# Performance work log

Measured on AMD Instinct MI355X. Metric: run time of the kernel, lower is better.

The kernel has to match this reference:

```python
import jax, jax.numpy as jnp
import numpy as np

N5, N4, N3, K = 10242, 2562, 642, 7  # icosphere node counts (levels 5,4,3), spatial kernel size
M = 32  # mchannel
EPS = 1e-8


def _sconv(x, neigh, W, b, relu=True):
    # x: [B,T,N,Cin]; neigh: [N,K] 1-ring indices; W: [K,Cin,Cout]
    xn = x[:, :, neigh, :]                        # [B,T,N,K,Cin] irregular gather
    y = jnp.einsum('btnkc,kcd->btnd', xn, W) + b  # per-node kernel contraction
    return jax.nn.relu(y) if relu else y


def _spool(x, pidx):
    # max-pool fine->coarse mesh: pidx [Ncoarse,Kp] indexes fine nodes
    return jnp.max(x[:, :, pidx, :], axis=3)


def _unpool(x, uidx):
    # coarse->fine copy: uidx [Nfine] indexes coarse nodes
    return x[:, :, uidx, :]


def _cos(f, a):
    # torch.nn.CosineSimilarity(dim=-1): dot / max(|f|*|a|, eps)
    dot = jnp.sum(f * a, axis=-1)
    nf = jnp.linalg.norm(f, axis=-1)
    na = jnp.linalg.norm(a, axis=-1)
    return dot / jnp.maximum(nf * na, EPS)


def setup_inputs() -> dict:
    key = jax.random.key(0)
    ks = jax.random.split(key, 32)
    w = lambda i, shape: jax.random.normal(ks[i], shape, jnp.float32) * 0.05
    inp = {
        'frame': jax.random.normal(ks[0], (1, 16, N5, 3), jnp.float32),
        'aem': jax.random.normal(ks[1], (1, 16, N5), jnp.float32),
        'W0f': w(2, (K, 3, M)),        'b0f': w(3, (M,)),
        'W0a': w(4, (K, 1, M)),        'b0a': w(5, (M,)),
        'W1f': w(6, (K, M, 2 * M)),    'b1f': w(7, (2 * M,)),
        'W1a': w(8, (K, M, 2 * M)),    'b1a': w(9, (2 * M,)),
        'W2f': w(10, (K, 2 * M, 4 * M)), 'b2f': w(11, (4 * M,)),
        'W2a': w(12, (K, 2 * M, 4 * M)), 'b2a': w(13, (4 * M,)),
        'W7': w(14, (K, 12 * M, 2 * M)), 'b7': w(15, (2 * M,)),
        'W8': w(16, (K, 4 * M, M)),    'b8': w(17, (M,)),
        'W9': w(18, (K, M, 1)),        'b9': w(19, (1,)),
        'neigh5': jax.random.randint(ks[20], (N5, K), 0, N5),
        'neigh4': jax.random.randint(ks[21], (N4, K), 0, N4),
        'neigh3': jax.random.randint(ks[22], (N3, K), 0, N3),
        'pool5': jax.random.randint(ks[23], (N4, K), 0, N5),
        'pool4': jax.random.randint(ks[24], (N3, K), 0, N4),
        'up4': jax.random.randint(ks[25], (N4,), 0, N3),
        'up5': jax.random.randint(ks[26], (N5,), 0, N4),
        'Tlocation': jax.random.randint(ks[27], (1, 16), 0, 16),
    }
    return inp


def reference(frame, aem, W0f, b0f, W0a, b0a, W1f, b1f, W1a, b1a, W2f, b2f,
              W2a, b2a, W7, b7, W8, b8, W9, b9,
              neigh5, neigh4, neigh3, pool5, pool4, up4, up5, Tlocation):
    a = aem[..., None]                                    # [B,T,N5,1]
    # encoder level 0 (N5)
    c0f = _sconv(frame, neigh5, W0f, b0f)
    c0a = _sconv(a, neigh5, W0a, b0a)
    p0f = _spool(c0f, pool5)
    p0a = _spool(c0a, pool5)
    m0 = _cos(c0f, c0a)[..., None]                        # [B,T,N5,1]
    c0f_att, c0a_att = c0f * m0, c0a * m0
    # encoder level 1 (N4)
    c1f = _sconv(p0f, neigh4, W1f, b1f)
    c1a = _sconv(p0a, neigh4, W1a, b1a)
    p1f = _spool(c1f, pool4)
    p1a = _spool(c1a, pool4)
    m1 = _cos(c1f, c1a)[..., None]
    c1f_att, c1a_att = c1f * m1, c1a * m1
    # bottleneck (N3)
    c2f = _sconv(p1f, neigh3, W2f, b2f)
    c2a = _sconv(p1a, neigh3, W2a, b2a)
    m2 = _cos(c2f, c2a)[..., None]
    conv2 = jnp.concatenate((c2f * m2, c2a * m2), axis=-1)  # [B,T,N3,8M]
    # decoder
    cat7 = jnp.concatenate((_unpool(conv2, up4), c1f_att, c1a_att), axis=-1)  # [B,T,N4,12M]
    conv7 = _sconv(cat7, neigh4, W7, b7)
    cat8 = jnp.concatenate((_unpool(conv7, up5), c0f_att, c0a_att), axis=-1)  # [B,T,N5,4M]
    conv8 = _sconv(cat8, neigh5, W8, b8)
    conv9 = _sconv(conv8, neigh5, W9, b9, relu=False)[..., 0]  # [B,T,N5]
    return jax.nn.softmax(conv9, axis=-1)
```

## Files before the change

kernel.cpp:

```cpp
#include <hip/hip_runtime.h>
#include <cfloat>
#include <cstdint>


constexpr int T  = 16;
constexpr int n5 = 10242, n4 = 2562, n3 = 642;
constexpr int K  = 7;

using bf16x8 = __attribute__((ext_vector_type(8))) short;
using f32x4  = __attribute__((ext_vector_type(4))) float;

static __device__ __forceinline__ float bf2f(unsigned short u) {
    return __uint_as_float((unsigned)u << 16);
}
static __device__ __forceinline__ unsigned short f2bf(float x) {
    unsigned u = __float_as_uint(x);
    u += 0x7FFF + ((u >> 16) & 1);
    return (unsigned short)(u >> 16);
}

__global__ __launch_bounds__(256) void conv0_kernel(
    const float* __restrict__ frame, const float* __restrict__ aem,
    const float* __restrict__ W0f, const float* __restrict__ b0f,
    const float* __restrict__ W0a, const float* __restrict__ b0a,
    const int* __restrict__ neigh5,
    unsigned short* __restrict__ c0f, unsigned short* __restrict__ c0a,
    unsigned short* __restrict__ att0)
{
    const int g = threadIdx.x >> 5;
    const int d = threadIdx.x & 31;
    const int per_t = (n5 + 7) / 8;
    const int t = blockIdx.x / per_t;
    const int n = (blockIdx.x % per_t) * 8 + g;
    if (n >= n5) return;

    float accf = b0f[d];
    float acca = b0a[d];
    const int* nb = neigh5 + n * K;
    #pragma unroll
    for (int k = 0; k < K; ++k) {
        const int j = nb[k];
        const float* fr = frame + ((size_t)t * n5 + j) * 3;
        const float av = aem[(size_t)t * n5 + j];
        accf = fmaf(fr[0], W0f[(k * 3 + 0) * 32 + d], accf);
        accf = fmaf(fr[1], W0f[(k * 3 + 1) * 32 + d], accf);
        accf = fmaf(fr[2], W0f[(k * 3 + 2) * 32 + d], accf);
        acca = fmaf(av, W0a[k * 32 + d], acca);
    }
    accf = fmaxf(accf, 0.f);
    acca = fmaxf(acca, 0.f);

    float dot = accf * acca, ff = accf * accf, aa = acca * acca;
    #pragma unroll
    for (int m = 1; m < 32; m <<= 1) {
        dot += __shfl_xor(dot, m, 32);
        ff  += __shfl_xor(ff,  m, 32);
        aa  += __shfl_xor(aa,  m, 32);
    }
    const float mm = dot / fmaxf(sqrtf(ff) * sqrtf(aa), 1e-8f);
    const size_t base = ((size_t)t * n5 + n) * 32;
    c0f[base + d] = f2bf(accf);
    c0a[base + d] = f2bf(acca);
    const size_t abase = ((size_t)t * n5 + n) * 64;
    att0[abase + d]      = f2bf(accf * mm);
    att0[abase + 32 + d] = f2bf(acca * mm);
}

template<int C>
__global__ __launch_bounds__(256) void pool_kernel(
    const unsigned short* __restrict__ in, const int* __restrict__ pidx,
    int Nin, int Nout, unsigned short* __restrict__ out)
{
    constexpr int C8 = C / 8;
    const int idx = blockIdx.x * 256 + threadIdx.x;
    if (idx >= T * Nout * C8) return;
    const int c8 = idx % C8;
    const int n  = (idx / C8) % Nout;
    const int t  = idx / (C8 * Nout);
    const int* pp = pidx + n * K;
    float m[8];
    #pragma unroll
    for (int j = 0; j < 8; ++j) m[j] = -FLT_MAX;
    #pragma unroll
    for (int k = 0; k < K; ++k) {
        const uint4 v = reinterpret_cast<const uint4*>(in)[((size_t)t * Nin + pp[k]) * C8 + c8];
        const unsigned short* s = reinterpret_cast<const unsigned short*>(&v);
        #pragma unroll
        for (int j = 0; j < 8; ++j) m[j] = fmaxf(m[j], bf2f(s[j]));
    }
    unsigned short o[8];
    #pragma unroll
    for (int j = 0; j < 8; ++j) o[j] = f2bf(m[j]);
    reinterpret_cast<uint4*>(out)[((size_t)t * Nout + n) * C8 + c8] =
        *reinterpret_cast<const uint4*>(o);
}

template<int C, int NN>
__global__ __launch_bounds__(256) void cosatt_kernel(
    const unsigned short* __restrict__ f, const unsigned short* __restrict__ a,
    unsigned short* __restrict__ att)
{
    constexpr int CPL = C / 64;
    const int w = threadIdx.x >> 6, lane = threadIdx.x & 63;
    const int idx = blockIdx.x * 4 + w;
    if (idx >= T * NN) return;
    const unsigned short* fr = f + (size_t)idx * C;
    const unsigned short* ar = a + (size_t)idx * C;
    float xs[CPL], ys[CPL];
    float dot = 0.f, ff = 0.f, aa = 0.f;
    #pragma unroll
    for (int i = 0; i < CPL; ++i) {
        const float x = bf2f(fr[lane + i * 64]);
        const float y = bf2f(ar[lane + i * 64]);
        xs[i] = x; ys[i] = y;
        dot = fmaf(x, y, dot);
        ff  = fmaf(x, x, ff);
        aa  = fmaf(y, y, aa);
    }
    #pragma unroll
    for (int msk = 1; msk < 64; msk <<= 1) {
        dot += __shfl_xor(dot, msk);
        ff  += __shfl_xor(ff,  msk);
        aa  += __shfl_xor(aa,  msk);
    }
    const float m = dot / fmaxf(sqrtf(ff) * sqrtf(aa), 1e-8f);
    unsigned short* orow = att + (size_t)idx * 2 * C;
    #pragma unroll
    for (int i = 0; i < CPL; ++i) {
        orow[lane + i * 64]     = f2bf(xs[i] * m);
        orow[C + lane + i * 64] = f2bf(ys[i] * m);
    }
}

struct PlainB16 {
    const uint4* x; int N; int C8;
    struct Ref { int o; };
    __device__ __forceinline__ Ref prep(int t, int node) const {
        return { (int)(((size_t)t * N + node) * C8) };
    }
    __device__ __forceinline__ uint4 chunk(const Ref& r, int c8) const {
        return x[r.o + c8];
    }
};

struct Cat7B16 {
    const uint4* att2; const uint4* att1; const int* up4;
    __device__ __forceinline__ uint4 row8(int t, int node, int c8) const {
        if (c8 < 32)
            return att2[((size_t)t * n3 + up4[node]) * 32 + c8];
        return att1[((size_t)t * n4 + node) * 16 + (c8 - 32)];
    }
};

struct Cat8B16 {
    const uint4* cv7; const uint4* att0; const int* up5;
    __device__ __forceinline__ uint4 row8(int t, int node, int c8) const {
        if (c8 < 8)
            return cv7[((size_t)t * n4 + up5[node]) * 8 + c8];
        return att0[((size_t)t * n5 + node) * 8 + (c8 - 8)];
    }
};

__global__ __launch_bounds__(256) void wprep_all_kernel(
    const float* __restrict__ W1f, const float* __restrict__ W1a,
    const float* __restrict__ W2f, const float* __restrict__ W2a,
    const float* __restrict__ W7,  const float* __restrict__ W8,
    unsigned short* __restrict__ Wt1f, unsigned short* __restrict__ Wt1a,
    unsigned short* __restrict__ Wt2f, unsigned short* __restrict__ Wt2a,
    unsigned short* __restrict__ Wt7,  unsigned short* __restrict__ Wt8)
{
    int idx = blockIdx.x * 256 + threadIdx.x;
    const float* W; unsigned short* Wt; int KCv, CO;
    if (idx < 14336)       { W = W1f; Wt = Wt1f; KCv = 224;  CO = 64;  }
    else if (idx < 28672)  { idx -= 14336;  W = W1a; Wt = Wt1a; KCv = 224;  CO = 64;  }
    else if (idx < 86016)  { idx -= 28672;  W = W2f; Wt = Wt2f; KCv = 448;  CO = 128; }
    else if (idx < 143360) { idx -= 86016;  W = W2a; Wt = Wt2a; KCv = 448;  CO = 128; }
    else if (idx < 315392) { idx -= 143360; W = W7;  Wt = Wt7;  KCv = 2688; CO = 64;  }
    else                   { idx -= 315392; W = W8;  Wt = Wt8;  KCv = 896;  CO = 32;  }
    const int d = idx / KCv, kc = idx - d * KCv;
    Wt[idx] = f2bf(W[(size_t)kc * CO + d]);
}

template<int CIN, int COUT, int BM, class Loader>
__global__ __launch_bounds__(256) void gemm_zp_kernel(
    Loader ldr, int N, int Mt,
    const unsigned short* __restrict__ Wt,
    unsigned short* __restrict__ Z)
{
    constexpr int KC    = K * CIN;
    constexpr int BK    = 64;
    constexpr int KSTEPS = CIN / BK;
    constexpr int U4R   = BK / 8;
    constexpr int WGR_N = COUT / 32;
    constexpr int WGR_M = 4 / WGR_N;
    constexpr int VPTA  = BM * U4R / 256;
    constexpr int VPTW  = COUT * U4R / 256;
    static_assert(BM == WGR_M * 32 && CIN % BK == 0 && VPTW >= 1 && BM * COUT <= BM * BK);

    __shared__ __align__(16) unsigned short As[BM * BK];
    __shared__ __align__(16) unsigned short Ws[COUT * BK];

    const int xcd = blockIdx.x & 7;
    int rest = blockIdx.x >> 3;
    const int half = Mt * K;
    const int hi = (rest >= half) ? 1 : 0;
    const int t  = 2 * xcd + hi;
    const int j  = rest - hi * half;
    const int tile_m = j / K;
    const int kk_    = j % K;

    const int tid = threadIdx.x, lane = tid & 63, wave = tid >> 6;
    const int wr = wave / WGR_N, wc = wave % WGR_N;
    const int l15 = lane & 15, lhi = lane >> 4;
    const int m0 = tile_m * BM;

    f32x4 acc[2][2] = {};

    for (int ks = 0; ks < KSTEPS; ++ks) {
        uint4 av[VPTA];
        #pragma unroll
        for (int v = 0; v < VPTA; ++v) {
            const int g = tid + v * 256, row = g / U4R, c8 = g % U4R;
            av[v] = ldr.row8(t, min(m0 + row, N - 1), ks * U4R + c8);
        }
        uint4 wv[VPTW];
        #pragma unroll
        for (int v = 0; v < VPTW; ++v) {
            const int g = tid + v * 256, d = g / U4R, c8 = g % U4R;
            wv[v] = *reinterpret_cast<const uint4*>(
                Wt + (size_t)d * KC + kk_ * CIN + ks * BK + c8 * 8);
        }

        __syncthreads();
        #pragma unroll
        for (int v = 0; v < VPTA; ++v) {
            const int g = tid + v * 256, row = g / U4R, c8 = g % U4R;
            *reinterpret_cast<uint4*>(&As[(row * BK + c8 * 8) ^ ((row & 7) << 3)]) = av[v];
        }
        #pragma unroll
        for (int v = 0; v < VPTW; ++v) {
            const int g = tid + v * 256, d = g / U4R, c8 = g % U4R;
            *reinterpret_cast<uint4*>(&Ws[(d * BK + c8 * 8) ^ ((d & 7) << 3)]) = wv[v];
        }
        __syncthreads();

        #pragma unroll
        for (int kk2 = 0; kk2 < 2; ++kk2) {
            const int kb = kk2 * 32 + lhi * 8;
            bf16x8 a[2], b[2];
            #pragma unroll
            for (int m = 0; m < 2; ++m) {
                const int row = wr * 32 + m * 16 + l15;
                a[m] = *reinterpret_cast<const bf16x8*>(&As[(row * BK + kb) ^ ((row & 7) << 3)]);
            }
            #pragma unroll
            for (int n = 0; n < 2; ++n) {
                const int col = wc * 32 + n * 16 + l15;
                b[n] = *reinterpret_cast<const bf16x8*>(&Ws[(col * BK + kb) ^ ((col & 7) << 3)]);
            }
            #pragma unroll
            for (int m = 0; m < 2; ++m)
                #pragma unroll
                for (int n = 0; n < 2; ++n)
                    acc[m][n] = __builtin_amdgcn_mfma_f32_16x16x32_bf16(a[m], b[n], acc[m][n], 0, 0, 0);
        }
    }

    __syncthreads();
    unsigned short* Cs = As;
    #pragma unroll
    for (int n = 0; n < 2; ++n) {
        const int col = wc * 32 + n * 16 + l15;
        #pragma unroll
        for (int m = 0; m < 2; ++m)
            #pragma unroll
            for (int i = 0; i < 4; ++i)
                Cs[(wr * 32 + m * 16 + lhi * 4 + i) * COUT + col] = f2bf(acc[m][n][i]);
    }
    __syncthreads();
    constexpr int RPT = COUT / 8;
    constexpr int CV  = BM * COUT / 8 / 256;
    #pragma unroll
    for (int v = 0; v < CV; ++v) {
        const int g = tid + v * 256, row = g / RPT, c8 = g % RPT;
        const int grow = m0 + row;
        if (grow < N)
            *reinterpret_cast<uint4*>(
                &Z[(((size_t)kk_ * T + t) * N + grow) * COUT + c8 * 8]) =
                *reinterpret_cast<const uint4*>(&Cs[row * COUT + c8 * 8]);
    }
}

template<int COUT>
__global__ __launch_bounds__(256) void epi_p_kernel(
    const unsigned short* __restrict__ Z, const int* __restrict__ neigh,
    int N, int Bt, const float* __restrict__ bias, unsigned short* __restrict__ out)
{
    constexpr int C8 = COUT / 8;
    const int xcd = blockIdx.x & 7;
    int idx = blockIdx.x >> 3;
    const int hi = (idx >= Bt) ? 1 : 0;
    const int t  = 2 * xcd + hi;
    const int e  = (idx - hi * Bt) * 256 + threadIdx.x;
    if (e >= N * C8) return;
    const int c8 = e % C8;
    const int n  = e / C8;
    const int* nb = neigh + n * K;

    float s[8];
    #pragma unroll
    for (int j = 0; j < 8; ++j) s[j] = bias[c8 * 8 + j];
    #pragma unroll
    for (int k = 0; k < K; ++k) {
        const uint4 v = *reinterpret_cast<const uint4*>(
            &Z[(((size_t)k * T + t) * N + nb[k]) * COUT + c8 * 8]);
        const unsigned short* p = reinterpret_cast<const unsigned short*>(&v);
        #pragma unroll
        for (int j = 0; j < 8; ++j) s[j] += bf2f(p[j]);
    }
    unsigned short o[8];
    #pragma unroll
    for (int j = 0; j < 8; ++j) o[j] = f2bf(fmaxf(s[j], 0.f));
    *reinterpret_cast<uint4*>(&out[((size_t)t * N + n) * COUT + c8 * 8]) =
        *reinterpret_cast<const uint4*>(o);
}

template<int CIN, int COUT, class Loader>
__device__ __forceinline__ void sconv_tile(
    const Loader& ldr, const int* __restrict__ neigh, int N, int t,
    int tile_m, int tile_n,
    const unsigned short* __restrict__ Wt, const float* __restrict__ bias,
    unsigned short* __restrict__ out)
{
    constexpr int KC     = K * CIN;
    constexpr int CHUNKS = CIN / 32;
    constexpr int STEPS  = K * CHUNKS;
    constexpr int D      = STEPS < 3 ? STEPS : 3;

    const int lane = threadIdx.x & 63;
    const int l15 = lane & 15, lhi = lane >> 4;

    const int r0 = tile_m * 32 + l15;
    const int row0 = min(r0, N - 1), row1 = min(r0 + 16, N - 1);

    typename Loader::Ref ref0[K], ref1[K];
    #pragma unroll
    for (int k = 0; k < K; ++k) {
        ref0[k] = ldr.prep(t, neigh[row0 * K + k]);
        ref1[k] = ldr.prep(t, neigh[row1 * K + k]);
    }

    const int col0 = tile_n * 32 + l15;
    const unsigned short* w0p = Wt + (size_t)col0 * KC + lhi * 8;
    const unsigned short* w1p = w0p + (size_t)16 * KC;

    uint4 qa0[D], qa1[D], qb0[D], qb1[D];

    auto issue = [&](int s, int slot) {
        const int k = s / CHUNKS, c = s - k * CHUNKS;
        const int c8 = c * 4 + lhi;
        qa0[slot] = ldr.chunk(ref0[k], c8);
        qa1[slot] = ldr.chunk(ref1[k], c8);
        qb0[slot] = *reinterpret_cast<const uint4*>(w0p + k * CIN + c * 32);
        qb1[slot] = *reinterpret_cast<const uint4*>(w1p + k * CIN + c * 32);
    };

    f32x4 acc[2][2] = {};

    #pragma unroll
    for (int s = 0; s < D; ++s) issue(s, s);
    __builtin_amdgcn_sched_barrier(0);

    #pragma unroll
    for (int s = 0; s < STEPS; ++s) {
        const int slot = s % D;
        const bf16x8 a0 = __builtin_bit_cast(bf16x8, qa0[slot]);
        const bf16x8 a1 = __builtin_bit_cast(bf16x8, qa1[slot]);
        const bf16x8 b0 = __builtin_bit_cast(bf16x8, qb0[slot]);
        const bf16x8 b1 = __builtin_bit_cast(bf16x8, qb1[slot]);
        acc[0][0] = __builtin_amdgcn_mfma_f32_16x16x32_bf16(a0, b0, acc[0][0], 0, 0, 0);
        acc[0][1] = __builtin_amdgcn_mfma_f32_16x16x32_bf16(a0, b1, acc[0][1], 0, 0, 0);
        acc[1][0] = __builtin_amdgcn_mfma_f32_16x16x32_bf16(a1, b0, acc[1][0], 0, 0, 0);
        acc[1][1] = __builtin_amdgcn_mfma_f32_16x16x32_bf16(a1, b1, acc[1][1], 0, 0, 0);
        if (s + D < STEPS) issue(s + D, slot);
        __builtin_amdgcn_sched_barrier(0);
    }

    #pragma unroll
    for (int n = 0; n < 2; ++n) {
        const int gcol = tile_n * 32 + n * 16 + l15;
        const float bv = bias[gcol];
        #pragma unroll
        for (int m = 0; m < 2; ++m) {
            #pragma unroll
            for (int i = 0; i < 4; ++i) {
                const int grow = tile_m * 32 + m * 16 + lhi * 4 + i;
                if (grow < N)
                    out[((size_t)t * N + grow) * COUT + gcol] =
                        f2bf(fmaxf(acc[m][n][i] + bv, 0.f));
            }
        }
    }
}

template<int CIN, int COUT, class Loader>
__global__ __launch_bounds__(64, 2) void sconv_rd2_kernel(
    Loader lf, Loader la, const int* __restrict__ neigh, int N, int U,
    const unsigned short* __restrict__ Wtf, const unsigned short* __restrict__ Wta,
    const float* __restrict__ bf_, const float* __restrict__ ba_,
    unsigned short* __restrict__ of_, unsigned short* __restrict__ oa_)
{
    constexpr int TN = COUT / 32;
    const int xcd = blockIdx.x & 7;
    int idx = blockIdx.x >> 3;
    const int sel = idx & 1; idx >>= 1;
    const int hi = (idx >= U) ? 1 : 0;
    const int t  = 2 * xcd + hi;
    const int w  = idx - hi * U;
    const Loader L = sel ? la : lf;
    const unsigned short* Wt = sel ? Wta : Wtf;
    const float* bias = sel ? ba_ : bf_;
    unsigned short* out = sel ? oa_ : of_;
    sconv_tile<CIN, COUT, Loader>(L, neigh, N, t, w / TN, w % TN, Wt, bias, out);
}

__global__ __launch_bounds__(256) void conv9_kernel(
    const unsigned short* __restrict__ cv8, const int* __restrict__ neigh5,
    const float* __restrict__ W9, const float* __restrict__ b9,
    float* __restrict__ logits)
{
    const int idx = blockIdx.x * 256 + threadIdx.x;
    if (idx >= T * n5) return;
    const int n = idx % n5;
    const int t = idx / n5;
    float acc = b9[0];
    const int* nb = neigh5 + n * K;
    #pragma unroll
    for (int k = 0; k < K; ++k) {
        const uint4* row = reinterpret_cast<const uint4*>(cv8 + ((size_t)t * n5 + nb[k]) * 32);
        const float* wk = W9 + k * 32;
        #pragma unroll
        for (int c4 = 0; c4 < 4; ++c4) {
            const uint4 v = row[c4];
            const unsigned short* s = reinterpret_cast<const unsigned short*>(&v);
            #pragma unroll
            for (int jj = 0; jj < 8; ++jj)
                acc = fmaf(bf2f(s[jj]), wk[c4 * 8 + jj], acc);
        }
    }
    logits[idx] = acc;
}

__global__ __launch_bounds__(1024) void softmax_kernel(
    const float* __restrict__ logits, float* __restrict__ out)
{
    const int t = blockIdx.x, tid = threadIdx.x;
    const float* x = logits + (size_t)t * n5;
    float* y = out + (size_t)t * n5;
    __shared__ float redmax[16], redsum[16];

    float mx = -FLT_MAX;
    for (int i = tid; i < n5; i += 1024) mx = fmaxf(mx, x[i]);
    #pragma unroll
    for (int m = 1; m < 64; m <<= 1) mx = fmaxf(mx, __shfl_xor(mx, m));
    if ((tid & 63) == 0) redmax[tid >> 6] = mx;
    __syncthreads();
    mx = redmax[0];
    #pragma unroll
    for (int i = 1; i < 16; ++i) mx = fmaxf(mx, redmax[i]);

    float s = 0.f;
    for (int i = tid; i < n5; i += 1024) s += expf(x[i] - mx);
    #pragma unroll
    for (int m = 1; m < 64; m <<= 1) s += __shfl_xor(s, m);
    if ((tid & 63) == 0) redsum[tid >> 6] = s;
    __syncthreads();
    s = 0.f;
    #pragma unroll
    for (int i = 0; i < 16; ++i) s += redsum[i];

    for (int i = tid; i < n5; i += 1024) y[i] = expf(x[i] - mx) / s;
}

extern "C" void kernel_launch(void* const* d_in, const int* in_sizes, int n_in,
                              void* d_out, int out_size, void* d_ws, size_t ws_size,
                              hipStream_t stream)
{
    const float* frame = (const float*)d_in[0];
    const float* aem   = (const float*)d_in[1];
    const float* W0f = (const float*)d_in[2];
    const float* b0f = (const float*)d_in[3];
    const float* W0a = (const float*)d_in[4];
    const float* b0a = (const float*)d_in[5];
    const float* W1f = (const float*)d_in[6];
    const float* b1f = (const float*)d_in[7];
    const float* W1a = (const float*)d_in[8];
    const float* b1a = (const float*)d_in[9];
    const float* W2f = (const float*)d_in[10];
    const float* b2f = (const float*)d_in[11];
    const float* W2a = (const float*)d_in[12];
    const float* b2a = (const float*)d_in[13];
    const float* W7  = (const float*)d_in[14];
    const float* b7  = (const float*)d_in[15];
    const float* W8  = (const float*)d_in[16];
    const float* b8  = (const float*)d_in[17];
    const float* W9  = (const float*)d_in[18];
    const float* b9  = (const float*)d_in[19];
    const int* neigh5 = (const int*)d_in[20];
    const int* neigh4 = (const int*)d_in[21];
    const int* neigh3 = (const int*)d_in[22];
    const int* pool5  = (const int*)d_in[23];
    const int* pool4  = (const int*)d_in[24];
    const int* up4    = (const int*)d_in[25];
    const int* up5    = (const int*)d_in[26];

    unsigned short* wsu = (unsigned short*)d_ws;
    size_t off = 0;
    auto ua = [&](size_t n) {
        unsigned short* p = wsu + off; off += (n + 63) & ~(size_t)63; return p;
    };
    unsigned short* c0f  = ua((size_t)T * n5 * 32);
    unsigned short* c0a  = ua((size_t)T * n5 * 32);
    unsigned short* att0 = ua((size_t)T * n5 * 64);
    unsigned short* p0f  = ua((size_t)T * n4 * 32);
    unsigned short* p0a  = ua((size_t)T * n4 * 32);
    unsigned short* c1f  = ua((size_t)T * n4 * 64);
    unsigned short* c1a  = ua((size_t)T * n4 * 64);
    unsigned short* att1 = ua((size_t)T * n4 * 128);
    unsigned short* p1f  = ua((size_t)T * n3 * 64);
    unsigned short* p1a  = ua((size_t)T * n3 * 64);
    unsigned short* c2f  = ua((size_t)T * n3 * 128);
    unsigned short* c2a  = ua((size_t)T * n3 * 128);
    unsigned short* att2 = ua((size_t)T * n3 * 256);
    unsigned short* cv7  = ua((size_t)T * n4 * 64);
    unsigned short* cv8  = ua((size_t)T * n5 * 32);
    unsigned short* Wt1f = ua((size_t)64 * 224);
    unsigned short* Wt1a = ua((size_t)64 * 224);
    unsigned short* Wt2f = ua((size_t)128 * 448);
    unsigned short* Wt2a = ua((size_t)128 * 448);
    unsigned short* Wt7  = ua((size_t)64 * 2688);
    unsigned short* Wt8  = ua((size_t)32 * 896);
    unsigned short* Zbuf = ua((size_t)K * T * n5 * 32);
    float* lgt = (float*)(wsu + ((off + 1) & ~(size_t)1));

    wprep_all_kernel<<<1344, 256, 0, stream>>>(
        W1f, W1a, W2f, W2a, W7, W8, Wt1f, Wt1a, Wt2f, Wt2a, Wt7, Wt8);

    conv0_kernel<<<T * ((n5 + 7) / 8), 256, 0, stream>>>(
        frame, aem, W0f, b0f, W0a, b0a, neigh5, c0f, c0a, att0);

    {
        const int thr = T * n4 * (32 / 8);
        pool_kernel<32><<<(thr + 255) / 256, 256, 0, stream>>>(c0f, pool5, n5, n4, p0f);
        pool_kernel<32><<<(thr + 255) / 256, 256, 0, stream>>>(c0a, pool5, n5, n4, p0a);
    }

    {
        constexpr int U = 81 * 2;
        sconv_rd2_kernel<32, 64><<<8 * 4 * U, 64, 0, stream>>>(
            PlainB16{(const uint4*)p0f, n4, 4}, PlainB16{(const uint4*)p0a, n4, 4},
            neigh4, n4, U, Wt1f, Wt1a, b1f, b1a, c1f, c1a);
    }
    cosatt_kernel<64, n4><<<(T * n4 + 3) / 4, 256, 0, stream>>>(c1f, c1a, att1);

    {
        const int thr = T * n3 * (64 / 8);
        pool_kernel<64><<<(thr + 255) / 256, 256, 0, stream>>>(c1f, pool4, n4, n3, p1f);
        pool_kernel<64><<<(thr + 255) / 256, 256, 0, stream>>>(c1a, pool4, n4, n3, p1a);
    }

    {
        constexpr int U = 21 * 4;
        sconv_rd2_kernel<64, 128><<<8 * 4 * U, 64, 0, stream>>>(
            PlainB16{(const uint4*)p1f, n3, 8}, PlainB16{(const uint4*)p1a, n3, 8},
            neigh3, n3, U, Wt2f, Wt2a, b2f, b2a, c2f, c2a);
    }
    cosatt_kernel<128, n3><<<(T * n3 + 3) / 4, 256, 0, stream>>>(c2f, c2a, att2);

    {
        constexpr int Mt = (n4 + 63) / 64;
        gemm_zp_kernel<384, 64, 64><<<16 * Mt * K, 256, 0, stream>>>(
            Cat7B16{(const uint4*)att2, (const uint4*)att1, up4}, n4, Mt, Wt7, Zbuf);
        constexpr int Bt = (n4 * 8 + 255) / 256;
        epi_p_kernel<64><<<8 * 2 * Bt, 256, 0, stream>>>(
            Zbuf, neigh4, n4, Bt, b7, cv7);
    }

    {
        constexpr int Mt = (n5 + 127) / 128;
        gemm_zp_kernel<128, 32, 128><<<16 * Mt * K, 256, 0, stream>>>(
            Cat8B16{(const uint4*)cv7, (const uint4*)att0, up5}, n5, Mt, Wt8, Zbuf);
        constexpr int Bt = (n5 * 4 + 255) / 256;
        epi_p_kernel<32><<<8 * 2 * Bt, 256, 0, stream>>>(
            Zbuf, neigh5, n5, Bt, b8, cv8);
    }

    conv9_kernel<<<(T * n5 + 255) / 256, 256, 0, stream>>>(cv8, neigh5, W9, b9, lgt);

    softmax_kernel<<<T, 1024, 0, stream>>>(lgt, (float*)d_out);
}
```

Measured before the change: 265.4 us.

## Stage activation tile once in LDS and loop over all kernel taps per block

The gather-then-GEMM kernels for conv7 and conv8 now load the whole activation tile (all Cin) into shared memory once per block and loop over the seven kernel taps inside the block. Previously each tap was a separate block that reloaded the same activation rows. Weights are now read straight from global memory into registers instead of being staged through LDS. This cuts redundant gather traffic and the grid size by a factor of K, at the cost of more LDS per block (lower occupancy for CIN=384), fewer blocks, and uncoalesced, uncached-in-LDS weight loads.

```diff
diff --git a/kernel.cpp b/kernel.cpp
--- a/kernel.cpp
+++ b/kernel.cpp
@@ -145,19 +145,25 @@
 
 struct Cat7B16 {
     const uint4* att2; const uint4* att1; const int* up4;
-    __device__ __forceinline__ uint4 row8(int t, int node, int c8) const {
-        if (c8 < 32)
-            return att2[((size_t)t * n3 + up4[node]) * 32 + c8];
-        return att1[((size_t)t * n4 + node) * 16 + (c8 - 32)];
+    struct Ref { int o2, o1; };
+    __device__ __forceinline__ Ref prep(int t, int node) const {
+        return { (int)(((size_t)t * n3 + up4[node]) * 32),
+                 (int)(((size_t)t * n4 + node) * 16) };
+    }
+    __device__ __forceinline__ uint4 chunk(const Ref& r, int c8) const {
+        return (c8 < 32) ? att2[r.o2 + c8] : att1[r.o1 + (c8 - 32)];
     }
 };
 
 struct Cat8B16 {
     const uint4* cv7; const uint4* att0; const int* up5;
-    __device__ __forceinline__ uint4 row8(int t, int node, int c8) const {
-        if (c8 < 8)
-            return cv7[((size_t)t * n4 + up5[node]) * 8 + c8];
-        return att0[((size_t)t * n5 + node) * 8 + (c8 - 8)];
+    struct Ref { int o7, o0; };
+    __device__ __forceinline__ Ref prep(int t, int node) const {
+        return { (int)(((size_t)t * n4 + up5[node]) * 8),
+                 (int)(((size_t)t * n5 + node) * 8) };
+    }
+    __device__ __forceinline__ uint4 chunk(const Ref& r, int c8) const {
+        return (c8 < 8) ? cv7[r.o7 + c8] : att0[r.o0 + (c8 - 8)];
     }
 };
 
@@ -182,112 +188,103 @@
 }
 
 template<int CIN, int COUT, int BM, class Loader>
-__global__ __launch_bounds__(256) void gemm_zp_kernel(
+__global__ __launch_bounds__(256) void gemm_kk_kernel(
     Loader ldr, int N, int Mt,
     const unsigned short* __restrict__ Wt,
     unsigned short* __restrict__ Z)
 {
-    constexpr int KC    = K * CIN;
-    constexpr int BK    = 64;
+    constexpr int KC     = K * CIN;
+    constexpr int BK     = 64;
     constexpr int KSTEPS = CIN / BK;
-    constexpr int U4R   = BK / 8;
-    constexpr int WGR_N = COUT / 32;
-    constexpr int WGR_M = 4 / WGR_N;
-    constexpr int VPTA  = BM * U4R / 256;
-    constexpr int VPTW  = COUT * U4R / 256;
-    static_assert(BM == WGR_M * 32 && CIN % BK == 0 && VPTW >= 1 && BM * COUT <= BM * BK);
-
-    __shared__ __align__(16) unsigned short As[BM * BK];
-    __shared__ __align__(16) unsigned short Ws[COUT * BK];
+    constexpr int U4R    = BK / 8;
+    constexpr int WGR_N  = COUT / 32;
+    constexpr int WGR_M  = 4 / WGR_N;
+    constexpr int VPTA   = BM * U4R / 256;
+    static_assert(BM == WGR_M * 32 && CIN % BK == 0);
+
+    __shared__ __align__(16) unsigned short As[KSTEPS][BM * BK];
+    __shared__ __align__(16) unsigned short Cs[BM * COUT];
 
     const int xcd = blockIdx.x & 7;
-    int rest = blockIdx.x >> 3;
-    const int half = Mt * K;
-    const int hi = (rest >= half) ? 1 : 0;
+    int idx = blockIdx.x >> 3;
+    const int hi = (idx >= Mt) ? 1 : 0;
     const int t  = 2 * xcd + hi;
-    const int j  = rest - hi * half;
-    const int tile_m = j / K;
-    const int kk_    = j % K;
+    const int tile_m = idx - hi * Mt;
+    const int m0 = tile_m * BM;
 
     const int tid = threadIdx.x, lane = tid & 63, wave = tid >> 6;
     const int wr = wave / WGR_N, wc = wave % WGR_N;
     const int l15 = lane & 15, lhi = lane >> 4;
-    const int m0 = tile_m * BM;
-
-    f32x4 acc[2][2] = {};
-
+
+    typename Loader::Ref ref[VPTA];
+    #pragma unroll
+    for (int v = 0; v < VPTA; ++v) {
+        const int row = (tid + v * 256) / U4R;
+        ref[v] = ldr.prep(t, min(m0 + row, N - 1));
+    }
+    #pragma unroll
     for (int ks = 0; ks < KSTEPS; ++ks) {
-        uint4 av[VPTA];
         #pragma unroll
         for (int v = 0; v < VPTA; ++v) {
             const int g = tid + v * 256, row = g / U4R, c8 = g % U4R;
-            av[v] = ldr.row8(t, min(m0 + row, N - 1), ks * U4R + c8);
+            const uint4 av = ldr.chunk(ref[v], ks * U4R + c8);
+            *reinterpret_cast<uint4*>(&As[ks][(row * BK + c8 * 8) ^ ((row & 7) << 3)]) = av;
         }
-        uint4 wv[VPTW];
-        #pragma unroll
-        for (int v = 0; v < VPTW; ++v) {
-            const int g = tid + v * 256, d = g / U4R, c8 = g % U4R;
-            wv[v] = *reinterpret_cast<const uint4*>(
-                Wt + (size_t)d * KC + kk_ * CIN + ks * BK + c8 * 8);
+    }
+
+    const unsigned short* w0p = Wt + (size_t)(wc * 32 + l15) * KC + lhi * 8;
+    const unsigned short* w1p = w0p + (size_t)16 * KC;
+
+    __syncthreads();
+
+    for (int kk = 0; kk < K; ++kk) {
+        f32x4 acc[2][2] = {};
+        #pragma unroll
+        for (int ks = 0; ks < KSTEPS; ++ks) {
+            #pragma unroll
+            for (int kk2 = 0; kk2 < 2; ++kk2) {
+                const int kb = kk2 * 32 + lhi * 8;
+                bf16x8 a[2], b[2];
+                #pragma unroll
+                for (int m = 0; m < 2; ++m) {
+                    const int row = wr * 32 + m * 16 + l15;
+                    a[m] = *reinterpret_cast<const bf16x8*>(
+                        &As[ks][(row * BK + kb) ^ ((row & 7) << 3)]);
+                }
+                const int woff = kk * CIN + ks * BK + kk2 * 32;
+                b[0] = *reinterpret_cast<const bf16x8*>(w0p + woff);
+                b[1] = *reinterpret_cast<const bf16x8*>(w1p + woff);
+                #pragma unroll
+                for (int m = 0; m < 2; ++m)
+                    #pragma unroll
+                    for (int n = 0; n < 2; ++n)
+                        acc[m][n] = __builtin_amdgcn_mfma_f32_16x16x32_bf16(
+                            a[m], b[n], acc[m][n], 0, 0, 0);
+            }
         }
 
         __syncthreads();
         #pragma unroll
-        for (int v = 0; v < VPTA; ++v) {
-            const int g = tid + v * 256, row = g / U4R, c8 = g % U4R;
-            *reinterpret_cast<uint4*>(&As[(row * BK + c8 * 8) ^ ((row & 7) << 3)]) = av[v];
-        }
-        #pragma unroll
-        for (int v = 0; v < VPTW; ++v) {
-            const int g = tid + v * 256, d = g / U4R, c8 = g % U4R;
-            *reinterpret_cast<uint4*>(&Ws[(d * BK + c8 * 8) ^ ((d & 7) << 3)]) = wv[v];
-        }
-        __syncthreads();
-
-        #pragma unroll
-        for (int kk2 = 0; kk2 < 2; ++kk2) {
-            const int kb = kk2 * 32 + lhi * 8;
-            bf16x8 a[2], b[2];
-            #pragma unroll
-            for (int m = 0; m < 2; ++m) {
-                const int row = wr * 32 + m * 16 + l15;
-                a[m] = *reinterpret_cast<const bf16x8*>(&As[(row * BK + kb) ^ ((row & 7) << 3)]);
-            }
-            #pragma unroll
-            for (int n = 0; n < 2; ++n) {
-                const int col = wc * 32 + n * 16 + l15;
-                b[n] = *reinterpret_cast<const bf16x8*>(&Ws[(col * BK + kb) ^ ((col & 7) << 3)]);
-            }
+        for (int n = 0; n < 2; ++n) {
+            const int col = wc * 32 + n * 16 + l15;
             #pragma unroll
             for (int m = 0; m < 2; ++m)
                 #pragma unroll
-                for (int n = 0; n < 2; ++n)
-                    acc[m][n] = __builtin_amdgcn_mfma_f32_16x16x32_bf16(a[m], b[n], acc[m][n], 0, 0, 0);
+                for (int i = 0; i < 4; ++i)
+                    Cs[(wr * 32 + m * 16 + lhi * 4 + i) * COUT + col] = f2bf(acc[m][n][i]);
         }
-    }
-
-    __syncthreads();
-    unsigned short* Cs = As;
-    #pragma unroll
-    for (int n = 0; n < 2; ++n) {
-        const int col = wc * 32 + n * 16 + l15;
-        #pragma unroll
-        for (int m = 0; m < 2; ++m)
-            #pragma unroll
-            for (int i = 0; i < 4; ++i)
-                Cs[(wr * 32 + m * 16 + lhi * 4 + i) * COUT + col] = f2bf(acc[m][n][i]);
-    }
-    __syncthreads();
-    constexpr int RPT = COUT / 8;
-    constexpr int CV  = BM * COUT / 8 / 256;
-    #pragma unroll
-    for (int v = 0; v < CV; ++v) {
-        const int g = tid + v * 256, row = g / RPT, c8 = g % RPT;
-        const int grow = m0 + row;
-        if (grow < N)
-            *reinterpret_cast<uint4*>(
-                &Z[(((size_t)kk_ * T + t) * N + grow) * COUT + c8 * 8]) =
-                *reinterpret_cast<const uint4*>(&Cs[row * COUT + c8 * 8]);
+        __syncthreads();
+        constexpr int RPT = COUT / 8;
+        constexpr int CV  = BM * COUT / 8 / 256;
+        #pragma unroll
+        for (int v = 0; v < CV; ++v) {
+            const int g = tid + v * 256, row = g / RPT, c8 = g % RPT;
+            const int grow = m0 + row;
+            if (grow < N)
+                *reinterpret_cast<uint4*>(
+                    &Z[(((size_t)kk * T + t) * N + grow) * COUT + c8 * 8]) =
+                    *reinterpret_cast<const uint4*>(&Cs[row * COUT + c8 * 8]);
+        }
     }
 }
 
@@ -579,7 +576,7 @@
 
     {
         constexpr int Mt = (n4 + 63) / 64;
-        gemm_zp_kernel<384, 64, 64><<<16 * Mt * K, 256, 0, stream>>>(
+        gemm_kk_kernel<384, 64, 64><<<16 * Mt, 256, 0, stream>>>(
             Cat7B16{(const uint4*)att2, (const uint4*)att1, up4}, n4, Mt, Wt7, Zbuf);
         constexpr int Bt = (n4 * 8 + 255) / 256;
         epi_p_kernel<64><<<8 * 2 * Bt, 256, 0, stream>>>(
@@ -588,7 +585,7 @@
 
     {
         constexpr int Mt = (n5 + 127) / 128;
-        gemm_zp_kernel<128, 32, 128><<<16 * Mt * K, 256, 0, stream>>>(
+        gemm_kk_kernel<128, 32, 128><<<16 * Mt, 256, 0, stream>>>(
             Cat8B16{(const uint4*)cv7, (const uint4*)att0, up5}, n5, Mt, Wt8, Zbuf);
         constexpr int Bt = (n5 * 4 + 255) / 256;
         epi_p_kernel<32><<<8 * 2 * Bt, 256, 0, stream>>>(
```

Result: slower. 292.9 us (+10.4%).
